# Optimization experiments

Measured on AMD Instinct MI355X. Metric: run time of the kernel, lower is better.

## Reference

```python
import jax, jax.numpy as jnp
import numpy as np

N, E, F_IN, HID, HEADS, OUT = 50000, 800000, 128, 64, 4, 40


def gat_layer(x, src, dst, n, W, a_src, a_dst, b, heads, ch):
    # PyG GATConv: h = x @ W per head; e_ij = LeakyReLU(a_src.h_j + a_dst.h_i)
    h = (x @ W).reshape(n, heads, ch)
    al_s = jnp.einsum('nhc,hc->nh', h, a_src)  # source-side logit term
    al_d = jnp.einsum('nhc,hc->nh', h, a_dst)  # target-side logit term
    e = jax.nn.leaky_relu(al_s[src] + al_d[dst], negative_slope=0.2)  # [E,H]
    m = jax.ops.segment_max(e, dst, num_segments=n)  # stable softmax per target node
    e = jnp.exp(e - m[dst])
    s = jax.ops.segment_sum(e, dst, num_segments=n)
    alpha = e / s[dst]  # [E,H]
    out = jax.ops.segment_sum(h[src] * alpha[:, :, None], dst, num_segments=n)  # [n,H,C]
    return out.reshape(n, heads * ch) + b


def gat_forward(x, src, dst, W0, as0, ad0, b0, W1, as1, ad1, b1, W2, as2, ad2, b2):
    n = x.shape[0]
    x = jax.nn.elu(gat_layer(x, src, dst, n, W0, as0, ad0, b0, HEADS, HID))
    x = jax.nn.elu(gat_layer(x, src, dst, n, W1, as1, ad1, b1, HEADS, HID))
    x = gat_layer(x, src, dst, n, W2, as2, ad2, b2, 1, OUT)
    return jax.nn.log_softmax(x, axis=1)


def setup_inputs() -> dict:
    key = jax.random.key(0)
    ks = jax.random.split(key, 16)
    x = jax.random.normal(ks[0], (N, F_IN), dtype=jnp.float32)
    edge_index = jax.random.randint(ks[1], (2, E), 0, N, dtype=jnp.int64)
    g = lambda k, sh: jax.random.normal(k, sh, dtype=jnp.float32) * (1.0 / np.sqrt(sh[0]))
    d_hid = HID * HEADS
    return {
        'x': x, 'edge_index': edge_index,
        'W0': g(ks[2], (F_IN, d_hid)), 'as0': g(ks[3], (HEADS, HID)), 'ad0': g(ks[4], (HEADS, HID)), 'b0': jnp.zeros((d_hid,), jnp.float32),
        'W1': g(ks[5], (d_hid, d_hid)), 'as1': g(ks[6], (HEADS, HID)), 'ad1': g(ks[7], (HEADS, HID)), 'b1': jnp.zeros((d_hid,), jnp.float32),
        'W2': g(ks[8], (d_hid, OUT)), 'as2': g(ks[9], (1, OUT)), 'ad2': g(ks[10], (1, OUT)), 'b2': jnp.zeros((OUT,), jnp.float32),
    }


def reference(x, edge_index, W0, as0, ad0, b0, W1, as1, ad1, b1, W2, as2, ad2, b2):
    n = x.shape[0]
    loops = jnp.arange(n, dtype=edge_index.dtype)  # PyG add_self_loops=True
    src = jnp.concatenate([edge_index[0], loops])
    dst = jnp.concatenate([edge_index[1], loops])
    return gat_forward(x, src, dst, W0, as0, ad0, b0, W1, as1, ad1, b1, W2, as2, ad2, b2)
```

## Files before the change

### kernel.cpp

```cpp
#include <hip/hip_runtime.h>
#include <hip/hip_fp16.h>
#include <math.h>

#define NODES 50000
#define NEDGES 800000
#define TOT_E (NEDGES + NODES)
#define SCAN_B 256
#define SCAN_NB ((NODES + SCAN_B - 1) / SCAN_B)

typedef __attribute__((ext_vector_type(8))) _Float16 half8v;
typedef __attribute__((ext_vector_type(4))) float f32x4;

union U2H { uint u; __half2 h; };

static __device__ __forceinline__ float lrelu(float z) {
  return z > 0.f ? z : 0.2f * z;
}
static __device__ __forceinline__ ushort f2h(float f) {
  __half h = __float2half_rn(f);
  return *reinterpret_cast<ushort*>(&h);
}
static __device__ __forceinline__ void wave_lds_fence() {
  __builtin_amdgcn_wave_barrier();
  asm volatile("s_waitcnt lgkmcnt(0)" ::: "memory");
  __builtin_amdgcn_sched_barrier(0);
}

static __device__ __forceinline__ void packB_one(const float* __restrict__ W,
    ushort* __restrict__ Bp, int N, int NF, int idx) {
  int i = idx & 7;
  int lane = (idx >> 3) & 63;
  int rem = idx >> 9;
  int nf = rem % NF;
  int kf = rem / NF;
  int k = kf * 32 + (lane >> 4) * 8 + i;
  int col = nf * 16 + (lane & 15);
  float v = (col < N) ? W[(size_t)k * N + col] : 0.f;
  Bp[idx] = f2h(v);
}

__global__ __launch_bounds__(256) void k_setup(const int* __restrict__ dst,
    int* __restrict__ counts, const float* __restrict__ x, ushort* __restrict__ xb0,
    const float* __restrict__ W0, ushort* __restrict__ Bp0,
    const float* __restrict__ W1, ushort* __restrict__ Bp1,
    const float* __restrict__ W2, ushort* __restrict__ Bp2) {
  int gb = blockIdx.x;
  int tid = threadIdx.x;
  if (gb < 2048) {
    int stride = 2048 * 256;
    for (int i = gb * 256 + tid; i < TOT_E; i += stride) {
      int d = (i < NEDGES) ? dst[i] : (i - NEDGES);
      atomicAdd(&counts[d], 1);
    }
  } else if (gb < 4048) {
    int total4 = NODES * 128 / 4;
    int stride = 2000 * 256;
    for (int i = (gb - 2048) * 256 + tid; i < total4; i += stride) {
      float4 v = *(const float4*)&x[i * 4];
      ushort4 o;
      o.x = f2h(v.x); o.y = f2h(v.y); o.z = f2h(v.z); o.w = f2h(v.w);
      *(ushort4*)&xb0[i * 4] = o;
    }
  } else {
    int b = gb - 4048;
    int stride = 48 * 256;
    int base = b * 256 + tid;
    for (int idx = base; idx < 4 * 16 * 512; idx += stride) packB_one(W0, Bp0, 256, 16, idx);
    for (int idx = base; idx < 8 * 16 * 512; idx += stride) packB_one(W1, Bp1, 256, 16, idx);
    for (int idx = base; idx < 8 * 3 * 512; idx += stride)  packB_one(W2, Bp2, 40, 3, idx);
  }
}

__global__ __launch_bounds__(SCAN_B) void k_scan_red_part(const int* __restrict__ counts,
    int* __restrict__ bsum, int* __restrict__ bpre, int* __restrict__ done) {
  __shared__ int sm[SCAN_B];
  __shared__ int lastflag;
  int idx = blockIdx.x * SCAN_B + threadIdx.x;
  int v = (idx < NODES) ? counts[idx] : 0;
  sm[threadIdx.x] = v;
  __syncthreads();
  for (int off = SCAN_B / 2; off > 0; off >>= 1) {
    if (threadIdx.x < off) sm[threadIdx.x] += sm[threadIdx.x + off];
    __syncthreads();
  }
  if (threadIdx.x == 0) {
    __hip_atomic_store(&bsum[blockIdx.x], sm[0], __ATOMIC_RELEASE, __HIP_MEMORY_SCOPE_AGENT);
    int t = __hip_atomic_fetch_add(done, 1, __ATOMIC_ACQ_REL, __HIP_MEMORY_SCOPE_AGENT);
    lastflag = (t == (int)gridDim.x - 1);
  }
  __syncthreads();
  if (!lastflag) return;
  int tid = threadIdx.x;
  int b = (tid < SCAN_NB)
      ? __hip_atomic_load(&bsum[tid], __ATOMIC_ACQUIRE, __HIP_MEMORY_SCOPE_AGENT) : 0;
  __syncthreads();
  sm[tid] = b;
  __syncthreads();
  for (int off = 1; off < 256; off <<= 1) {
    int t2 = (tid >= off) ? sm[tid - off] : 0;
    __syncthreads();
    sm[tid] += t2;
    __syncthreads();
  }
  if (tid < SCAN_NB) bpre[tid] = sm[tid] - b;
}

__global__ __launch_bounds__(SCAN_B) void k_scan_emit(const int* __restrict__ counts,
    const int* __restrict__ bpre, int* __restrict__ offs, int* __restrict__ cur) {
  __shared__ int sm[SCAN_B];
  int idx = blockIdx.x * SCAN_B + threadIdx.x;
  int tid = threadIdx.x;
  int v = (idx < NODES) ? counts[idx] : 0;
  sm[tid] = v;
  __syncthreads();
  for (int off = 1; off < SCAN_B; off <<= 1) {
    int t = (tid >= off) ? sm[tid - off] : 0;
    __syncthreads();
    sm[tid] += t;
    __syncthreads();
  }
  int base = bpre[blockIdx.x];
  int excl = base + sm[tid] - v;
  if (idx < NODES) { offs[idx] = excl; cur[idx] = excl; }
  if (idx == NODES - 1) offs[NODES] = excl + v;
}

__global__ void k_scatter(const int* __restrict__ src, const int* __restrict__ dst,
                          int* __restrict__ cur, ushort* __restrict__ ssrc) {
  int stride = gridDim.x * blockDim.x;
  for (int i = blockIdx.x * blockDim.x + threadIdx.x; i < TOT_E; i += stride) {
    int s, d;
    if (i < NEDGES) { s = src[i]; d = dst[i]; } else { s = i - NEDGES; d = s; }
    int pos = atomicAdd(&cur[d], 1);
    ssrc[pos] = (ushort)s;
  }
}

template<int KF, int NFW, int CG, int HEADS, int NF_TOT>
__global__ __launch_bounds__(256, 2) void k_gemm_reg(
    const ushort* __restrict__ A, const ushort* __restrict__ Bp,
    ushort* __restrict__ H, const float* __restrict__ a_s, const float* __restrict__ a_d,
    float* __restrict__ al_s, float* __restrict__ al_d, int M, int N, int K) {
  int wib = threadIdx.x >> 6;
  int lane = threadIdx.x & 63;
  int lg = lane >> 4;
  int lr = lane & 15;
  int cg, strip0, sstride;
  if (CG == 4) { cg = wib; strip0 = blockIdx.x; sstride = gridDim.x; }
  else { cg = 0; strip0 = blockIdx.x * 4 + wib; sstride = gridDim.x * 4; }

  half8v b[KF][NFW];
#pragma unroll
  for (int kf = 0; kf < KF; ++kf)
#pragma unroll
    for (int n = 0; n < NFW; ++n)
      b[kf][n] = *(const half8v*)(Bp + ((size_t)(kf * NF_TOT + cg * NFW + n) * 64 + lane) * 8);

  float asc[NFW], adc[NFW];
#pragma unroll
  for (int n = 0; n < NFW; ++n) {
    int col = (cg * NFW + n) * 16 + lr;
    bool ok = col < N;
    asc[n] = ok ? a_s[col] : 0.f;
    adc[n] = ok ? a_d[col] : 0.f;
  }

  int nstrips = M >> 4;
  for (int strip = strip0; strip < nstrips; strip += sstride) {
    const ushort* arow = A + (size_t)(strip * 16 + lr) * K + lg * 8;
    half8v a[KF];
#pragma unroll
    for (int kf = 0; kf < KF; ++kf) a[kf] = *(const half8v*)(arow + kf * 32);
    f32x4 acc[NFW];
#pragma unroll
    for (int n = 0; n < NFW; ++n) acc[n] = (f32x4){0.f, 0.f, 0.f, 0.f};
#pragma unroll
    for (int kf = 0; kf < KF; ++kf)
#pragma unroll
      for (int n = 0; n < NFW; ++n)
        acc[n] = __builtin_amdgcn_mfma_f32_16x16x32_f16(a[kf], b[kf][n], acc[n], 0, 0, 0);

#pragma unroll
    for (int n = 0; n < NFW; ++n) {
      int col = (cg * NFW + n) * 16 + lr;
      if (col < N) {
#pragma unroll
        for (int r = 0; r < 4; ++r) {
          int row = strip * 16 + lg * 4 + r;
          H[(size_t)row * N + col] = f2h(acc[n][r]);
        }
      }
    }

    float ps[4], pd[4];
#pragma unroll
    for (int r = 0; r < 4; ++r) {
      float s = 0.f, d = 0.f;
#pragma unroll
      for (int n = 0; n < NFW; ++n) {
        s += acc[n][r] * asc[n];
        d += acc[n][r] * adc[n];
      }
      ps[r] = s; pd[r] = d;
    }
#pragma unroll
    for (int off = 1; off <= 8; off <<= 1)
#pragma unroll
      for (int t = 0; t < 4; ++t) {
        ps[t] += __shfl_xor(ps[t], off);
        pd[t] += __shfl_xor(pd[t], off);
      }
    if (lr < 4) {
      int row = strip * 16 + lg * 4 + lr;
      if (HEADS == 4) {
        al_s[row * 4 + cg] = ps[lr];
        al_d[row * 4 + cg] = pd[lr];
      } else {
        al_s[row] = ps[lr];
        al_d[row] = pd[lr];
      }
    }
  }
}

__global__ __launch_bounds__(256) void k_agg4(const ushort* __restrict__ hb,
    const float* __restrict__ al_s, const float* __restrict__ al_d,
    const int* __restrict__ offs, const ushort* __restrict__ ssrc,
    const float* __restrict__ bias, ushort* __restrict__ outb) {
  __shared__ uint s_sv[8][32];
  __shared__ uint s_al[8][2][33];
  int bid = blockIdx.x;
  int xcd = bid & 7;
  int hp = xcd >> 2;
  int nb = (bid >> 3) * 4 + (xcd & 3);
  int hw = threadIdx.x >> 5;
  int node = nb * 8 + hw;
  if (node >= NODES) return;
  int l = threadIdx.x & 31;
  int beg = offs[node], end = offs[node + 1];
  float2 ald2 = *(const float2*)&al_d[node * 4 + hp * 2];

  float m0 = -1e30f, m1 = -1e30f;
  for (int i = beg + l; i < end; i += 32) {
    int sv = ssrc[i];
    float2 a2 = *(const float2*)&al_s[sv * 4 + hp * 2];
    m0 = fmaxf(m0, lrelu(a2.x + ald2.x));
    m1 = fmaxf(m1, lrelu(a2.y + ald2.y));
  }
#pragma unroll
  for (int off = 1; off <= 16; off <<= 1) {
    m0 = fmaxf(m0, __shfl_xor(m0, off));
    m1 = fmaxf(m1, __shfl_xor(m1, off));
  }

  int e = l >> 4;
  int c = l & 15;
  int hsel = c >> 3;
  uint clb = (uint)(hp * 128 + c * 8);
  float sacc0 = 0.f, sacc1 = 0.f;
  __half2 z2 = __float2half2_rn(0.f);
  __half2 accA[4] = {z2, z2, z2, z2};
  __half2 accB[4] = {z2, z2, z2, z2};

  for (int cb = beg; cb < end; cb += 32) {
    int cnt = min(32, end - cb);
    wave_lds_fence();
    if (l < cnt) {
      uint sv = (uint)ssrc[cb + l];
      float2 a2 = *(const float2*)&al_s[sv * 4 + hp * 2];
      float t0 = __expf(lrelu(a2.x + ald2.x) - m0);
      float t1 = __expf(lrelu(a2.y + ald2.y) - m1);
      sacc0 += t0; sacc1 += t1;
      U2H p0, p1;
      p0.h = __float2half2_rn(t0); p1.h = __float2half2_rn(t1);
      s_sv[hw][l] = sv;
      s_al[hw][0][l] = p0.u; s_al[hw][1][l] = p1.u;
    }
    wave_lds_fence();
    int ee = e;
    for (; ee + 6 < cnt; ee += 8) {
      uint sv0 = s_sv[hw][ee],     sv1 = s_sv[hw][ee + 2];
      uint sv2 = s_sv[hw][ee + 4], sv3 = s_sv[hw][ee + 6];
      U2H a0, a1, a2, a3;
      a0.u = s_al[hw][hsel][ee];     a1.u = s_al[hw][hsel][ee + 2];
      a2.u = s_al[hw][hsel][ee + 4]; a3.u = s_al[hw][hsel][ee + 6];
      uint4 hv0 = *(const uint4*)(hb + ((sv0 << 8) + clb));
      uint4 hv1 = *(const uint4*)(hb + ((sv1 << 8) + clb));
      uint4 hv2 = *(const uint4*)(hb + ((sv2 << 8) + clb));
      uint4 hv3 = *(const uint4*)(hb + ((sv3 << 8) + clb));
      U2H v;
      v.u = hv0.x; accA[0] = __hfma2(a0.h, v.h, accA[0]);
      v.u = hv0.y; accA[1] = __hfma2(a0.h, v.h, accA[1]);
      v.u = hv0.z; accA[2] = __hfma2(a0.h, v.h, accA[2]);
      v.u = hv0.w; accA[3] = __hfma2(a0.h, v.h, accA[3]);
      v.u = hv1.x; accB[0] = __hfma2(a1.h, v.h, accB[0]);
      v.u = hv1.y; accB[1] = __hfma2(a1.h, v.h, accB[1]);
      v.u = hv1.z; accB[2] = __hfma2(a1.h, v.h, accB[2]);
      v.u = hv1.w; accB[3] = __hfma2(a1.h, v.h, accB[3]);
      v.u = hv2.x; accA[0] = __hfma2(a2.h, v.h, accA[0]);
      v.u = hv2.y; accA[1] = __hfma2(a2.h, v.h, accA[1]);
      v.u = hv2.z; accA[2] = __hfma2(a2.h, v.h, accA[2]);
      v.u = hv2.w; accA[3] = __hfma2(a2.h, v.h, accA[3]);
      v.u = hv3.x; accB[0] = __hfma2(a3.h, v.h, accB[0]);
      v.u = hv3.y; accB[1] = __hfma2(a3.h, v.h, accB[1]);
      v.u = hv3.z; accB[2] = __hfma2(a3.h, v.h, accB[2]);
      v.u = hv3.w; accB[3] = __hfma2(a3.h, v.h, accB[3]);
    }
    for (; ee < cnt; ee += 2) {
      uint sv = s_sv[hw][ee];
      U2H a0; a0.u = s_al[hw][hsel][ee];
      uint4 hv = *(const uint4*)(hb + ((sv << 8) + clb));
      U2H v;
      v.u = hv.x; accA[0] = __hfma2(a0.h, v.h, accA[0]);
      v.u = hv.y; accA[1] = __hfma2(a0.h, v.h, accA[1]);
      v.u = hv.z; accA[2] = __hfma2(a0.h, v.h, accA[2]);
      v.u = hv.w; accA[3] = __hfma2(a0.h, v.h, accA[3]);
    }
  }
#pragma unroll
  for (int off = 1; off <= 16; off <<= 1) {
    sacc0 += __shfl_xor(sacc0, off);
    sacc1 += __shfl_xor(sacc1, off);
  }
  float invs = 1.f / (hsel ? sacc1 : sacc0);
  ushort4 ores[2];
#pragma unroll
  for (int j = 0; j < 4; ++j) {
    U2H t; t.h = __hadd2(accA[j], accB[j]);
    U2H o; o.u = __shfl_xor(t.u, 16);
    t.h = __hadd2(t.h, o.h);
    float lo = __low2float(t.h) * invs + bias[clb + j * 2];
    float hi = __high2float(t.h) * invs + bias[clb + j * 2 + 1];
    lo = lo > 0.f ? lo : __expf(lo) - 1.f;
    hi = hi > 0.f ? hi : __expf(hi) - 1.f;
    ((ushort*)ores)[j * 2]     = f2h(lo);
    ((ushort*)ores)[j * 2 + 1] = f2h(hi);
  }
  if (e == 0) {
    *(ushort4*)(outb + (size_t)node * 256 + clb)     = ores[0];
    *(ushort4*)(outb + (size_t)node * 256 + clb + 4) = ores[1];
  }
}

__global__ __launch_bounds__(256) void k_agg1(const ushort* __restrict__ hb,
    const float* __restrict__ al_s, const float* __restrict__ al_d,
    const int* __restrict__ offs, const ushort* __restrict__ ssrc,
    const float* __restrict__ bias, float* __restrict__ out) {
  __shared__ uint s_sv[8][32];
  __shared__ uint s_al[8][32];
  int hw = threadIdx.x >> 5;
  int node = (blockIdx.x * 256 + threadIdx.x) >> 5;
  if (node >= NODES) return;
  int l = threadIdx.x & 31;
  int beg = offs[node], end = offs[node + 1];
  float ald = al_d[node];

  float m = -1e30f;
  for (int i = beg + l; i < end; i += 32)
    m = fmaxf(m, lrelu(al_s[ssrc[i]] + ald));
#pragma unroll
  for (int off = 1; off <= 16; off <<= 1) m = fmaxf(m, __shfl_xor(m, off));

  int p = l >> 4;
  int cq = l & 15;
  bool act = cq < 10;
  uint cqb = (uint)cq * 4;
  float sacc = 0.f;
  __half2 z2 = __float2half2_rn(0.f);
  __half2 accA[2] = {z2, z2};
  __half2 accB[2] = {z2, z2};
  for (int cb = beg; cb < end; cb += 32) {
    int cnt = min(32, end - cb);
    wave_lds_fence();
    if (l < cnt) {
      uint sv = (uint)ssrc[cb + l];
      float t = __expf(lrelu(al_s[sv] + ald) - m);
      sacc += t;
      U2H pk; pk.h = __float2half2_rn(t);
      s_sv[hw][l] = sv;
      s_al[hw][l] = pk.u;
    }
    wave_lds_fence();
    int e = p;
    for (; e + 14 < cnt; e += 16) {
      uint sv0 = s_sv[hw][e],      sv1 = s_sv[hw][e + 2];
      uint sv2 = s_sv[hw][e + 4],  sv3 = s_sv[hw][e + 6];
      uint sv4 = s_sv[hw][e + 8],  sv5 = s_sv[hw][e + 10];
      uint sv6 = s_sv[hw][e + 12], sv7 = s_sv[hw][e + 14];
      U2H a0, a1, a2, a3, a4, a5, a6, a7;
      a0.u = s_al[hw][e];      a1.u = s_al[hw][e + 2];
      a2.u = s_al[hw][e + 4];  a3.u = s_al[hw][e + 6];
      a4.u = s_al[hw][e + 8];  a5.u = s_al[hw][e + 10];
      a6.u = s_al[hw][e + 12]; a7.u = s_al[hw][e + 14];
      if (act) {
        uint2 hv0 = *(const uint2*)(hb + (sv0 * 40u + cqb));
        uint2 hv1 = *(const uint2*)(hb + (sv1 * 40u + cqb));
        uint2 hv2 = *(const uint2*)(hb + (sv2 * 40u + cqb));
        uint2 hv3 = *(const uint2*)(hb + (sv3 * 40u + cqb));
        uint2 hv4 = *(const uint2*)(hb + (sv4 * 40u + cqb));
        uint2 hv5 = *(const uint2*)(hb + (sv5 * 40u + cqb));
        uint2 hv6 = *(const uint2*)(hb + (sv6 * 40u + cqb));
        uint2 hv7 = *(const uint2*)(hb + (sv7 * 40u + cqb));
        U2H v;
        v.u = hv0.x; accA[0] = __hfma2(a0.h, v.h, accA[0]);
        v.u = hv0.y; accA[1] = __hfma2(a0.h, v.h, accA[1]);
        v.u = hv1.x; accB[0] = __hfma2(a1.h, v.h, accB[0]);
        v.u = hv1.y; accB[1] = __hfma2(a1.h, v.h, accB[1]);
        v.u = hv2.x; accA[0] = __hfma2(a2.h, v.h, accA[0]);
        v.u = hv2.y; accA[1] = __hfma2(a2.h, v.h, accA[1]);
        v.u = hv3.x; accB[0] = __hfma2(a3.h, v.h, accB[0]);
        v.u = hv3.y; accB[1] = __hfma2(a3.h, v.h, accB[1]);
        v.u = hv4.x; accA[0] = __hfma2(a4.h, v.h, accA[0]);
        v.u = hv4.y; accA[1] = __hfma2(a4.h, v.h, accA[1]);
        v.u = hv5.x; accB[0] = __hfma2(a5.h, v.h, accB[0]);
        v.u = hv5.y; accB[1] = __hfma2(a5.h, v.h, accB[1]);
        v.u = hv6.x; accA[0] = __hfma2(a6.h, v.h, accA[0]);
        v.u = hv6.y; accA[1] = __hfma2(a6.h, v.h, accA[1]);
        v.u = hv7.x; accB[0] = __hfma2(a7.h, v.h, accB[0]);
        v.u = hv7.y; accB[1] = __hfma2(a7.h, v.h, accB[1]);
      }
    }
    for (; e + 6 < cnt; e += 8) {
      uint sv0 = s_sv[hw][e],     sv1 = s_sv[hw][e + 2];
      uint sv2 = s_sv[hw][e + 4], sv3 = s_sv[hw][e + 6];
      U2H a0, a1, a2, a3;
      a0.u = s_al[hw][e];     a1.u = s_al[hw][e + 2];
      a2.u = s_al[hw][e + 4]; a3.u = s_al[hw][e + 6];
      if (act) {
        uint2 hv0 = *(const uint2*)(hb + (sv0 * 40u + cqb));
        uint2 hv1 = *(const uint2*)(hb + (sv1 * 40u + cqb));
        uint2 hv2 = *(const uint2*)(hb + (sv2 * 40u + cqb));
        uint2 hv3 = *(const uint2*)(hb + (sv3 * 40u + cqb));
        U2H v;
        v.u = hv0.x; accA[0] = __hfma2(a0.h, v.h, accA[0]);
        v.u = hv0.y; accA[1] = __hfma2(a0.h, v.h, accA[1]);
        v.u = hv1.x; accB[0] = __hfma2(a1.h, v.h, accB[0]);
        v.u = hv1.y; accB[1] = __hfma2(a1.h, v.h, accB[1]);
        v.u = hv2.x; accA[0] = __hfma2(a2.h, v.h, accA[0]);
        v.u = hv2.y; accA[1] = __hfma2(a2.h, v.h, accA[1]);
        v.u = hv3.x; accB[0] = __hfma2(a3.h, v.h, accB[0]);
        v.u = hv3.y; accB[1] = __hfma2(a3.h, v.h, accB[1]);
      }
    }
    for (; e < cnt; e += 2) {
      uint sv = s_sv[hw][e];
      U2H a0; a0.u = s_al[hw][e];
      if (act) {
        uint2 hv = *(const uint2*)(hb + (sv * 40u + cqb));
        U2H v;
        v.u = hv.x; accA[0] = __hfma2(a0.h, v.h, accA[0]);
        v.u = hv.y; accA[1] = __hfma2(a0.h, v.h, accA[1]);
      }
    }
  }
#pragma unroll
  for (int off = 1; off <= 16; off <<= 1) sacc += __shfl_xor(sacc, off);
  float invs = 1.f / sacc;
  float vv[4];
#pragma unroll
  for (int j = 0; j < 2; ++j) {
    U2H t; t.h = __hadd2(accA[j], accB[j]);
    U2H o; o.u = __shfl_xor(t.u, 16);
    t.h = __hadd2(t.h, o.h);
    vv[j * 2]     = __low2float(t.h) * invs;
    vv[j * 2 + 1] = __high2float(t.h) * invs;
  }
  float mm = -1e30f;
  if (act) {
#pragma unroll
    for (int j = 0; j < 4; ++j) {
      vv[j] += bias[cq * 4 + j];
      mm = fmaxf(mm, vv[j]);
    }
  }
#pragma unroll
  for (int off = 1; off <= 8; off <<= 1) mm = fmaxf(mm, __shfl_xor(mm, off));
  float se = 0.f;
  if (act) {
#pragma unroll
    for (int j = 0; j < 4; ++j) se += __expf(vv[j] - mm);
  }
#pragma unroll
  for (int off = 1; off <= 8; off <<= 1) se += __shfl_xor(se, off);
  if (act && p == 0) {
    float lse = mm + __logf(se);
    float4 o;
    o.x = vv[0] - lse; o.y = vv[1] - lse; o.z = vv[2] - lse; o.w = vv[3] - lse;
    *(float4*)&out[(size_t)node * 40 + cq * 4] = o;
  }
}

extern "C" void kernel_launch(void* const* d_in, const int* in_sizes, int n_in,
                              void* d_out, int out_size, void* d_ws, size_t ws_size,
                              hipStream_t stream) {
  const float* x   = (const float*)d_in[0];
  const int*   ei  = (const int*)d_in[1];
  const float* W0  = (const float*)d_in[2];
  const float* as0 = (const float*)d_in[3];
  const float* ad0 = (const float*)d_in[4];
  const float* b0  = (const float*)d_in[5];
  const float* W1  = (const float*)d_in[6];
  const float* as1 = (const float*)d_in[7];
  const float* ad1 = (const float*)d_in[8];
  const float* b1  = (const float*)d_in[9];
  const float* W2  = (const float*)d_in[10];
  const float* as2 = (const float*)d_in[11];
  const float* ad2 = (const float*)d_in[12];
  const float* b2  = (const float*)d_in[13];
  float* out = (float*)d_out;

  char* p = (char*)d_ws;
  auto take = [&](size_t bytes) {
    char* q = p;
    p += (bytes + 255) & ~(size_t)255;
    return (void*)q;
  };
  ushort* xb0 = (ushort*)take((size_t)NODES * 128 * 2);
  ushort* xb1 = (ushort*)take((size_t)NODES * 256 * 2);
  ushort* xb2 = (ushort*)take((size_t)NODES * 256 * 2);
  ushort* hb  = (ushort*)take((size_t)NODES * 256 * 2);
  float* als  = (float*)take((size_t)NODES * 4 * 4);
  float* ald  = (float*)take((size_t)NODES * 4 * 4);
  ushort* ssrc= (ushort*)take((size_t)TOT_E * 2);
  int* offs   = (int*)take((size_t)(NODES + 1) * 4);
  int* cur    = (int*)take((size_t)NODES * 4);
  int* cnt    = (int*)take((size_t)(NODES + 64) * 4);
  int* done   = cnt + NODES;
  int* bsum   = (int*)take((size_t)SCAN_NB * 4);
  int* bpre   = (int*)take((size_t)SCAN_NB * 4);
  ushort* Bp0 = (ushort*)take((size_t)4 * 16 * 512 * 2);
  ushort* Bp1 = (ushort*)take((size_t)8 * 16 * 512 * 2);
  ushort* Bp2 = (ushort*)take((size_t)8 * 3 * 512 * 2);

  hipMemsetAsync(cnt, 0, (size_t)(NODES + 64) * 4, stream);
  k_setup<<<4096, 256, 0, stream>>>(ei + NEDGES, cnt, x, xb0, W0, Bp0, W1, Bp1, W2, Bp2);
  k_scan_red_part<<<SCAN_NB, SCAN_B, 0, stream>>>(cnt, bsum, bpre, done);
  k_scan_emit<<<SCAN_NB, SCAN_B, 0, stream>>>(cnt, bpre, offs, cur);
  k_scatter<<<4096, 256, 0, stream>>>(ei, ei + NEDGES, cur, ssrc);

  int nab = (NODES * 32 + 255) / 256;
  int nab4 = (nab + 3) & ~3;
  int nagg4 = nab4 * 2;

  k_gemm_reg<4, 4, 4, 4, 16><<<512, 256, 0, stream>>>(xb0, Bp0, hb, as0, ad0, als, ald, NODES, 256, 128);
  k_agg4<<<nagg4, 256, 0, stream>>>(hb, als, ald, offs, ssrc, b0, xb1);

  k_gemm_reg<8, 4, 4, 4, 16><<<512, 256, 0, stream>>>(xb1, Bp1, hb, as1, ad1, als, ald, NODES, 256, 256);
  k_agg4<<<nagg4, 256, 0, stream>>>(hb, als, ald, offs, ssrc, b1, xb2);

  k_gemm_reg<8, 3, 1, 1, 3><<<512, 256, 0, stream>>>(xb2, Bp2, hb, as2, ad2, als, ald, NODES, 40, 256);
  k_agg1<<<nab, 256, 0, stream>>>(hb, als, ald, offs, ssrc, b2, out);
}
```

Before: 287.9 us.

## Split 4-head aggregation into one head per block with 8-channel lanes

The attention aggregation kernel changes from each block covering a pair of heads (128 channels) to each block covering a single head (64 channels). The grid doubles, and the block-to-XCD mapping now groups nodes by head. Each 32-lane group handles 4 edges in parallel with 8 lanes per edge, so the per-edge softmax and logit work is computed once per head rather than twice. The trade-off is that every edge's source index and attention logit are now reloaded for each head, and the unroll depth per lane drops, which lowers memory-level parallelism.

```diff
diff --git a/kernel.cpp b/kernel.cpp
--- a/kernel.cpp
+++ b/kernel.cpp
@@ -228,36 +228,27 @@
     const int* __restrict__ offs, const ushort* __restrict__ ssrc,
     const float* __restrict__ bias, ushort* __restrict__ outb) {
   __shared__ uint s_sv[8][32];
-  __shared__ uint s_al[8][2][33];
+  __shared__ uint s_al[8][32];
   int bid = blockIdx.x;
-  int xcd = bid & 7;
-  int hp = xcd >> 2;
-  int nb = (bid >> 3) * 4 + (xcd & 3);
+  int head = (bid & 7) >> 1;
+  int nb = (bid >> 3) * 2 + (bid & 1);
   int hw = threadIdx.x >> 5;
   int node = nb * 8 + hw;
   if (node >= NODES) return;
   int l = threadIdx.x & 31;
   int beg = offs[node], end = offs[node + 1];
-  float2 ald2 = *(const float2*)&al_d[node * 4 + hp * 2];
-
-  float m0 = -1e30f, m1 = -1e30f;
-  for (int i = beg + l; i < end; i += 32) {
-    int sv = ssrc[i];
-    float2 a2 = *(const float2*)&al_s[sv * 4 + hp * 2];
-    m0 = fmaxf(m0, lrelu(a2.x + ald2.x));
-    m1 = fmaxf(m1, lrelu(a2.y + ald2.y));
-  }
-#pragma unroll
-  for (int off = 1; off <= 16; off <<= 1) {
-    m0 = fmaxf(m0, __shfl_xor(m0, off));
-    m1 = fmaxf(m1, __shfl_xor(m1, off));
-  }
-
-  int e = l >> 4;
-  int c = l & 15;
-  int hsel = c >> 3;
-  uint clb = (uint)(hp * 128 + c * 8);
-  float sacc0 = 0.f, sacc1 = 0.f;
+  float aldh = al_d[node * 4 + head];
+
+  float m = -1e30f;
+  for (int i = beg + l; i < end; i += 32)
+    m = fmaxf(m, lrelu(al_s[ssrc[i] * 4 + head] + aldh));
+#pragma unroll
+  for (int off = 1; off <= 16; off <<= 1) m = fmaxf(m, __shfl_xor(m, off));
+
+  int es = l >> 3;
+  int c = l & 7;
+  uint clb = (uint)(head * 64 + c * 8);
+  float sacc = 0.f;
   __half2 z2 = __float2half2_rn(0.f);
   __half2 accA[4] = {z2, z2, z2, z2};
   __half2 accB[4] = {z2, z2, z2, z2};
@@ -267,27 +258,20 @@
     wave_lds_fence();
     if (l < cnt) {
       uint sv = (uint)ssrc[cb + l];
-      float2 a2 = *(const float2*)&al_s[sv * 4 + hp * 2];
-      float t0 = __expf(lrelu(a2.x + ald2.x) - m0);
-      float t1 = __expf(lrelu(a2.y + ald2.y) - m1);
-      sacc0 += t0; sacc1 += t1;
-      U2H p0, p1;
-      p0.h = __float2half2_rn(t0); p1.h = __float2half2_rn(t1);
+      float t = __expf(lrelu(al_s[sv * 4 + head] + aldh) - m);
+      sacc += t;
+      U2H pk; pk.h = __float2half2_rn(t);
       s_sv[hw][l] = sv;
-      s_al[hw][0][l] = p0.u; s_al[hw][1][l] = p1.u;
+      s_al[hw][l] = pk.u;
     }
     wave_lds_fence();
-    int ee = e;
-    for (; ee + 6 < cnt; ee += 8) {
-      uint sv0 = s_sv[hw][ee],     sv1 = s_sv[hw][ee + 2];
-      uint sv2 = s_sv[hw][ee + 4], sv3 = s_sv[hw][ee + 6];
-      U2H a0, a1, a2, a3;
-      a0.u = s_al[hw][hsel][ee];     a1.u = s_al[hw][hsel][ee + 2];
-      a2.u = s_al[hw][hsel][ee + 4]; a3.u = s_al[hw][hsel][ee + 6];
+    int ee = es;
+    for (; ee + 7 < cnt; ee += 8) {
+      uint sv0 = s_sv[hw][ee], sv1 = s_sv[hw][ee + 4];
+      U2H a0, a1;
+      a0.u = s_al[hw][ee]; a1.u = s_al[hw][ee + 4];
       uint4 hv0 = *(const uint4*)(hb + ((sv0 << 8) + clb));
       uint4 hv1 = *(const uint4*)(hb + ((sv1 << 8) + clb));
-      uint4 hv2 = *(const uint4*)(hb + ((sv2 << 8) + clb));
-      uint4 hv3 = *(const uint4*)(hb + ((sv3 << 8) + clb));
       U2H v;
       v.u = hv0.x; accA[0] = __hfma2(a0.h, v.h, accA[0]);
       v.u = hv0.y; accA[1] = __hfma2(a0.h, v.h, accA[1]);
@@ -297,18 +281,10 @@
       v.u = hv1.y; accB[1] = __hfma2(a1.h, v.h, accB[1]);
       v.u = hv1.z; accB[2] = __hfma2(a1.h, v.h, accB[2]);
       v.u = hv1.w; accB[3] = __hfma2(a1.h, v.h, accB[3]);
-      v.u = hv2.x; accA[0] = __hfma2(a2.h, v.h, accA[0]);
-      v.u = hv2.y; accA[1] = __hfma2(a2.h, v.h, accA[1]);
-      v.u = hv2.z; accA[2] = __hfma2(a2.h, v.h, accA[2]);
-      v.u = hv2.w; accA[3] = __hfma2(a2.h, v.h, accA[3]);
-      v.u = hv3.x; accB[0] = __hfma2(a3.h, v.h, accB[0]);
-      v.u = hv3.y; accB[1] = __hfma2(a3.h, v.h, accB[1]);
-      v.u = hv3.z; accB[2] = __hfma2(a3.h, v.h, accB[2]);
-      v.u = hv3.w; accB[3] = __hfma2(a3.h, v.h, accB[3]);
-    }
-    for (; ee < cnt; ee += 2) {
+    }
+    for (; ee < cnt; ee += 4) {
       uint sv = s_sv[hw][ee];
-      U2H a0; a0.u = s_al[hw][hsel][ee];
+      U2H a0; a0.u = s_al[hw][ee];
       uint4 hv = *(const uint4*)(hb + ((sv << 8) + clb));
       U2H v;
       v.u = hv.x; accA[0] = __hfma2(a0.h, v.h, accA[0]);
@@ -318,17 +294,15 @@
     }
   }
 #pragma unroll
-  for (int off = 1; off <= 16; off <<= 1) {
-    sacc0 += __shfl_xor(sacc0, off);
-    sacc1 += __shfl_xor(sacc1, off);
-  }
-  float invs = 1.f / (hsel ? sacc1 : sacc0);
+  for (int off = 1; off <= 16; off <<= 1) sacc += __shfl_xor(sacc, off);
+  float invs = 1.f / sacc;
   ushort4 ores[2];
 #pragma unroll
   for (int j = 0; j < 4; ++j) {
     U2H t; t.h = __hadd2(accA[j], accB[j]);
-    U2H o; o.u = __shfl_xor(t.u, 16);
-    t.h = __hadd2(t.h, o.h);
+    U2H o;
+    o.u = __shfl_xor(t.u, 8);  t.h = __hadd2(t.h, o.h);
+    o.u = __shfl_xor(t.u, 16); t.h = __hadd2(t.h, o.h);
     float lo = __low2float(t.h) * invs + bias[clb + j * 2];
     float hi = __high2float(t.h) * invs + bias[clb + j * 2 + 1];
     lo = lo > 0.f ? lo : __expf(lo) - 1.f;
@@ -336,7 +310,7 @@
     ((ushort*)ores)[j * 2]     = f2h(lo);
     ((ushort*)ores)[j * 2 + 1] = f2h(hi);
   }
-  if (e == 0) {
+  if (es == 0) {
     *(ushort4*)(outb + (size_t)node * 256 + clb)     = ores[0];
     *(ushort4*)(outb + (size_t)node * 256 + clb + 4) = ores[1];
   }
@@ -539,8 +513,8 @@
   k_scatter<<<4096, 256, 0, stream>>>(ei, ei + NEDGES, cur, ssrc);
 
   int nab = (NODES * 32 + 255) / 256;
-  int nab4 = (nab + 3) & ~3;
-  int nagg4 = nab4 * 2;
+  int nab2 = (nab + 1) & ~1;
+  int nagg4 = nab2 * 4;
 
   k_gemm_reg<4, 4, 4, 4, 16><<<512, 256, 0, stream>>>(xb0, Bp0, hb, as0, ad0, als, ald, NODES, 256, 128);
   k_agg4<<<nagg4, 256, 0, stream>>>(hb, als, ald, offs, ssrc, b0, xb1);
```

Result: slower. 322.0 us (+11.8%).
